# Performance work log

Measured on AMD Instinct MI355X. Metric: run time of the kernel, lower is better.

Reference implementation:

```python
import jax, jax.numpy as jnp
import numpy as np

MD = 4  # max_displacement
NEG_SLOPE = 0.1  # LeakyReLU slope


def setup_inputs() -> dict:
    key = jax.random.key(0)
    k1, k2 = jax.random.split(key)
    B, H, W, C = 8, 128, 192, 128
    x1 = jax.random.normal(k1, (B, H, W, C), dtype=jnp.float32)
    warped = jax.random.normal(k2, (B, H, W, C), dtype=jnp.float32)
    return {"x1": x1, "warped": warped}


def reference(x1, warped):
    # cost[b,h,w,k] = mean_c x1[b,h,w,c] * warped[b,h+sh,w+sw,c]  (zero-padded)
    # k enumerates (sh, sw) in row-major order over [-MD, MD] x [-MD, MD].
    md = MD
    B, H, W, C = x1.shape
    wp = jnp.pad(warped, ((0, 0), (md, md), (md, md), (0, 0)))
    cv = []
    for sh in range(-md, md + 1):
        for sw in range(-md, md + 1):
            shifted = jax.lax.dynamic_slice(wp, (0, md + sh, md + sw, 0), (B, H, W, C))
            cv.append(jnp.mean(x1 * shifted, axis=3))
    cv = jnp.stack(cv, axis=3)  # [B, H, W, (2*md+1)**2]
    return jnp.where(cv >= 0, cv, NEG_SLOPE * cv)
```

## Files before the change

### kernel.cpp

```cpp
#include <hip/hip_runtime.h>


namespace {
constexpr int Bb = 8, Hh = 128, Ww = 192, Cn = 128;
constexpr int MDc = 4;
constexpr int TH = 8, TWT = 16;
constexpr int NTHR = 512;
constexpr int RH = 16;
constexpr int RPX = 24;
constexpr int KC = 32;
constexpr int NCH = Cn / KC;
constexpr int KQB = RPX * 16;
constexpr int ROWB = 4 * KQB;
constexpr int BUFB = RH * ROWB;
constexpr int RUNS = RH * RPX * 4;
constexpr int NIT = RUNS / NTHR;
constexpr float NEG = 0.1f;
}

typedef __fp16 h2v   __attribute__((ext_vector_type(2)));
typedef __fp16 f16x8 __attribute__((ext_vector_type(8)));
typedef float  f32x4 __attribute__((ext_vector_type(4)));

__device__ __forceinline__ unsigned pkh2(float a, float b) {
    h2v h = __builtin_amdgcn_cvt_pkrtz(a, b);
    return __builtin_bit_cast(unsigned, h);
}

__device__ __forceinline__ void barrier_lgkm() {
    asm volatile("s_waitcnt lgkmcnt(0)\n\ts_barrier" ::: "memory");
}

__global__ __launch_bounds__(NTHR, 4)
void costvol_mfma(const float* __restrict__ x1,
                  const float* __restrict__ wp,
                  float* __restrict__ out)
{
    __shared__ __align__(16) unsigned char smem[2 * BUFB];

    const int tid  = threadIdx.x;
    const int wv   = tid >> 6;
    const int lane = tid & 63;
    const int nI   = lane & 15;
    const int kq   = lane >> 4;

    const int id = blockIdx.x;
    const int wg = (id & 7) * 192 + (id >> 3);
    const int bx = wg % 12;
    const int t2 = wg / 12;
    const int by = t2 & 15;
    const int bz = t2 >> 4;

    const int w0 = bx * TWT;
    const int h0 = by * TH;
    const int b  = bz;

    int g_off[NIT]; int l_off[NIT]; bool g_ok[NIT];
#pragma unroll
    for (int it = 0; it < NIT; ++it) {
        int s   = tid + it * NTHR;
        int skq = s & 3;
        int t   = s >> 2;
        int px  = t % RPX;
        int row = t / RPX;
        int hw  = h0 - MDc + row;
        int ww  = w0 - MDc + px;
        bool ok = (unsigned)hw < (unsigned)Hh && (unsigned)ww < (unsigned)Ww;
        g_ok[it]  = ok;
        g_off[it] = ((b * Hh + (ok ? hw : 0)) * Ww + (ok ? ww : 0)) * Cn + skq * 8;
        l_off[it] = row * ROWB + skq * KQB + ((px ^ (skq << 1)) * 16);
    }

    uint4 gp[NIT];
    auto LOADCH = [&](int ch) {
#pragma unroll
        for (int it = 0; it < NIT; ++it) {
            if (g_ok[it]) {
                const float* p = wp + g_off[it] + ch * KC;
                float4 u = *reinterpret_cast<const float4*>(p);
                float4 v = *reinterpret_cast<const float4*>(p + 4);
                gp[it] = make_uint4(pkh2(u.x, u.y), pkh2(u.z, u.w),
                                    pkh2(v.x, v.y), pkh2(v.z, v.w));
            } else {
                gp[it] = make_uint4(0u, 0u, 0u, 0u);
            }
        }
    };
    auto WRITEB = [&](int buf) {
#pragma unroll
        for (int it = 0; it < NIT; ++it)
            *reinterpret_cast<uint4*>(smem + buf * BUFB + l_off[it]) = gp[it];
    };

    LOADCH(0);

    const float* xp = x1 + ((size_t)((b * Hh + h0 + wv) * Ww) + w0 + nI) * Cn + kq * 8;
    float4 ar_u, ar_v;
    ar_u = *reinterpret_cast<const float4*>(xp);
    ar_v = *reinterpret_cast<const float4*>(xp + 4);

    f32x4 ac0[9], ac1[9];
#pragma unroll
    for (int s = 0; s < 9; ++s) {
        f32x4 z = {0.f, 0.f, 0.f, 0.f};
        ac0[s] = z; ac1[s] = z;
    }

    const int ro0 = kq * KQB + ((nI ^ (kq << 1)) * 16);

    WRITEB(0); LOADCH(1);

    int cur = 0;
#pragma unroll
    for (int ch = 0; ch < NCH; ++ch) {
        barrier_lgkm();
        if (ch + 1 < NCH) WRITEB(cur ^ 1);
        if (ch + 2 < NCH) LOADCH(ch + 2);
        uint4 afr = make_uint4(pkh2(ar_u.x, ar_u.y), pkh2(ar_u.z, ar_u.w),
                               pkh2(ar_v.x, ar_v.y), pkh2(ar_v.z, ar_v.w));
        if (ch + 1 < NCH) {
            ar_u = *reinterpret_cast<const float4*>(xp + (ch + 1) * KC);
            ar_v = *reinterpret_cast<const float4*>(xp + (ch + 1) * KC + 4);
        }
        f16x8 av = __builtin_bit_cast(f16x8, afr);
        const unsigned char* base = smem + cur * BUFB;
#pragma unroll
        for (int sh = 0; sh < 9; ++sh) {
            const unsigned char* rp = base + (wv + sh) * ROWB;
            uint4 b0 = *reinterpret_cast<const uint4*>(rp + ro0);
            uint4 b1 = *reinterpret_cast<const uint4*>(rp + ro0 + 128);
            ac0[sh] = __builtin_amdgcn_mfma_f32_16x16x32_f16(
                av, __builtin_bit_cast(f16x8, b0), ac0[sh], 0, 0, 0);
            ac1[sh] = __builtin_amdgcn_mfma_f32_16x16x32_f16(
                av, __builtin_bit_cast(f16x8, b1), ac1[sh], 0, 0, 0);
        }
        cur ^= 1;
    }

    const float sc = 1.0f / (float)Cn;
    const size_t rowbase = ((size_t)((b * Hh + h0 + wv) * Ww) + w0) * 81;
#pragma unroll
    for (int rg = 0; rg < 4; ++rg) {
        int m = kq * 4 + rg;
        int d = nI - m;
        bool t0 = (d >= 0 && d <= 8);
        bool t1 = (d >= -8 && d <= 0 && nI >= 8);
        size_t mb = rowbase + (size_t)m * 81;
#pragma unroll
        for (int sh = 0; sh < 9; ++sh) {
            if (t0) {
                float v = ac0[sh][rg] * sc;
                v = (v >= 0.f) ? v : NEG * v;
                out[mb + sh * 9 + d] = v;
            }
            if (t1) {
                float v = ac1[sh][rg] * sc;
                v = (v >= 0.f) ? v : NEG * v;
                out[mb + sh * 9 + d + 8] = v;
            }
        }
    }
}

extern "C" void kernel_launch(void* const* d_in, const int* in_sizes, int n_in,
                              void* d_out, int out_size, void* d_ws, size_t ws_size,
                              hipStream_t stream) {
    const float* x1 = (const float*)d_in[0];
    const float* wp = (const float*)d_in[1];
    float* out = (float*)d_out;
    dim3 grid(12 * 16 * 8, 1, 1);
    costvol_mfma<<<grid, NTHR, 0, stream>>>(x1, wp, out);
}
```

Measured before the change: 59.65 us.

## Halve tile height and split vertical shifts across wave pairs

Tile height drops from 8 to 4 output rows, so the grid doubles. Each pair of waves now shares one output row, with one wave handling 5 vertical shifts and the other 4. The per-wave accumulator count falls from 18 to 10 MFMA tiles, which lowers register pressure and halves the shared-memory buffer, and so may raise occupancy and parallelism. In exchange, each block reloads a larger halo relative to its output (12 rows loaded for 4 output rows, against 16 for 8), which adds global-memory traffic. The two waves of a pair also do unequal work.

```diff
diff --git a/kernel.cpp b/kernel.cpp
--- a/kernel.cpp
+++ b/kernel.cpp
@@ -4,9 +4,9 @@
 namespace {
 constexpr int Bb = 8, Hh = 128, Ww = 192, Cn = 128;
 constexpr int MDc = 4;
-constexpr int TH = 8, TWT = 16;
+constexpr int TH = 4, TWT = 16;
 constexpr int NTHR = 512;
-constexpr int RH = 16;
+constexpr int RH = TH + 8;
 constexpr int RPX = 24;
 constexpr int KC = 32;
 constexpr int NCH = Cn / KC;
@@ -14,7 +14,7 @@
 constexpr int ROWB = 4 * KQB;
 constexpr int BUFB = RH * ROWB;
 constexpr int RUNS = RH * RPX * 4;
-constexpr int NIT = RUNS / NTHR;
+constexpr int NIT = 3;
 constexpr float NEG = 0.1f;
 }
 
@@ -39,17 +39,20 @@
     __shared__ __align__(16) unsigned char smem[2 * BUFB];
 
     const int tid  = threadIdx.x;
-    const int wv   = tid >> 6;
+    const int w    = tid >> 6;
+    const int wvr  = w >> 1;
+    const int shb  = (w & 1) * 5;
+    const int shn  = 5 - (w & 1);
     const int lane = tid & 63;
     const int nI   = lane & 15;
     const int kq   = lane >> 4;
 
     const int id = blockIdx.x;
-    const int wg = (id & 7) * 192 + (id >> 3);
+    const int wg = (id & 7) * 384 + (id >> 3);
     const int bx = wg % 12;
     const int t2 = wg / 12;
-    const int by = t2 & 15;
-    const int bz = t2 >> 4;
+    const int by = t2 & 31;
+    const int bz = t2 >> 5;
 
     const int w0 = bx * TWT;
     const int h0 = by * TH;
@@ -65,7 +68,8 @@
         int row = t / RPX;
         int hw  = h0 - MDc + row;
         int ww  = w0 - MDc + px;
-        bool ok = (unsigned)hw < (unsigned)Hh && (unsigned)ww < (unsigned)Ww;
+        bool ok = (s < RUNS) &&
+                  (unsigned)hw < (unsigned)Hh && (unsigned)ww < (unsigned)Ww;
         g_ok[it]  = ok;
         g_off[it] = ((b * Hh + (ok ? hw : 0)) * Ww + (ok ? ww : 0)) * Cn + skq * 8;
         l_off[it] = row * ROWB + skq * KQB + ((px ^ (skq << 1)) * 16);
@@ -87,21 +91,22 @@
         }
     };
     auto WRITEB = [&](int buf) {
-#pragma unroll
-        for (int it = 0; it < NIT; ++it)
-            *reinterpret_cast<uint4*>(smem + buf * BUFB + l_off[it]) = gp[it];
+        *reinterpret_cast<uint4*>(smem + buf * BUFB + l_off[0]) = gp[0];
+        *reinterpret_cast<uint4*>(smem + buf * BUFB + l_off[1]) = gp[1];
+        if (tid < RUNS - 2 * NTHR)
+            *reinterpret_cast<uint4*>(smem + buf * BUFB + l_off[2]) = gp[2];
     };
 
     LOADCH(0);
 
-    const float* xp = x1 + ((size_t)((b * Hh + h0 + wv) * Ww) + w0 + nI) * Cn + kq * 8;
+    const float* xp = x1 + ((size_t)((b * Hh + h0 + wvr) * Ww) + w0 + nI) * Cn + kq * 8;
     float4 ar_u, ar_v;
     ar_u = *reinterpret_cast<const float4*>(xp);
     ar_v = *reinterpret_cast<const float4*>(xp + 4);
 
-    f32x4 ac0[9], ac1[9];
+    f32x4 ac0[5], ac1[5];
 #pragma unroll
-    for (int s = 0; s < 9; ++s) {
+    for (int s = 0; s < 5; ++s) {
         f32x4 z = {0.f, 0.f, 0.f, 0.f};
         ac0[s] = z; ac1[s] = z;
     }
@@ -125,38 +130,42 @@
         f16x8 av = __builtin_bit_cast(f16x8, afr);
         const unsigned char* base = smem + cur * BUFB;
 #pragma unroll
-        for (int sh = 0; sh < 9; ++sh) {
-            const unsigned char* rp = base + (wv + sh) * ROWB;
-            uint4 b0 = *reinterpret_cast<const uint4*>(rp + ro0);
-            uint4 b1 = *reinterpret_cast<const uint4*>(rp + ro0 + 128);
-            ac0[sh] = __builtin_amdgcn_mfma_f32_16x16x32_f16(
-                av, __builtin_bit_cast(f16x8, b0), ac0[sh], 0, 0, 0);
-            ac1[sh] = __builtin_amdgcn_mfma_f32_16x16x32_f16(
-                av, __builtin_bit_cast(f16x8, b1), ac1[sh], 0, 0, 0);
+        for (int s = 0; s < 5; ++s) {
+            if (s < shn) {
+                const unsigned char* rp = base + (wvr + shb + s) * ROWB;
+                uint4 b0 = *reinterpret_cast<const uint4*>(rp + ro0);
+                uint4 b1 = *reinterpret_cast<const uint4*>(rp + ro0 + 128);
+                ac0[s] = __builtin_amdgcn_mfma_f32_16x16x32_f16(
+                    av, __builtin_bit_cast(f16x8, b0), ac0[s], 0, 0, 0);
+                ac1[s] = __builtin_amdgcn_mfma_f32_16x16x32_f16(
+                    av, __builtin_bit_cast(f16x8, b1), ac1[s], 0, 0, 0);
+            }
         }
         cur ^= 1;
     }
 
     const float sc = 1.0f / (float)Cn;
-    const size_t rowbase = ((size_t)((b * Hh + h0 + wv) * Ww) + w0) * 81;
+    const size_t rowbase = ((size_t)((b * Hh + h0 + wvr) * Ww) + w0) * 81;
 #pragma unroll
     for (int rg = 0; rg < 4; ++rg) {
         int m = kq * 4 + rg;
         int d = nI - m;
         bool t0 = (d >= 0 && d <= 8);
         bool t1 = (d >= -8 && d <= 0 && nI >= 8);
-        size_t mb = rowbase + (size_t)m * 81;
+        size_t mb = rowbase + (size_t)m * 81 + shb * 9;
 #pragma unroll
-        for (int sh = 0; sh < 9; ++sh) {
-            if (t0) {
-                float v = ac0[sh][rg] * sc;
-                v = (v >= 0.f) ? v : NEG * v;
-                out[mb + sh * 9 + d] = v;
-            }
-            if (t1) {
-                float v = ac1[sh][rg] * sc;
-                v = (v >= 0.f) ? v : NEG * v;
-                out[mb + sh * 9 + d + 8] = v;
+        for (int s = 0; s < 5; ++s) {
+            if (s < shn) {
+                if (t0) {
+                    float v = ac0[s][rg] * sc;
+                    v = (v >= 0.f) ? v : NEG * v;
+                    out[mb + s * 9 + d] = v;
+                }
+                if (t1) {
+                    float v = ac1[s][rg] * sc;
+                    v = (v >= 0.f) ? v : NEG * v;
+                    out[mb + s * 9 + d + 8] = v;
+                }
             }
         }
     }
@@ -168,6 +177,6 @@
     const float* x1 = (const float*)d_in[0];
     const float* wp = (const float*)d_in[1];
     float* out = (float*)d_out;
-    dim3 grid(12 * 16 * 8, 1, 1);
+    dim3 grid(12 * 32 * 8, 1, 1);
     costvol_mfma<<<grid, NTHR, 0, stream>>>(x1, wp, out);
 }
```

Measured after the change: 66.61 us. 1.12x slower.

## Make blocks persistent over three tiles with cross-tile prefetch pipelining

Applied to the files above, without the earlier changes.

Each block now processes three consecutive tiles instead of one, with the grid shrunk from 1536 to 512 blocks. The loads of the first chunks of the next tile are issued during the last chunks of the current tile, so global-load latency is overlapped across tile boundaries and per-block launch/prologue cost is amortized. The trade-off is fewer blocks, which reduces parallelism and occupancy slack for the 256 CUs (two blocks per CU), and adds register pressure from keeping the next tile's offsets live.

```diff
diff --git a/kernel.cpp b/kernel.cpp
--- a/kernel.cpp
+++ b/kernel.cpp
@@ -15,6 +15,7 @@
 constexpr int BUFB = RH * ROWB;
 constexpr int RUNS = RH * RPX * 4;
 constexpr int NIT = RUNS / NTHR;
+constexpr int NTILE = 3;
 constexpr float NEG = 0.1f;
 }
 
@@ -44,32 +45,36 @@
     const int nI   = lane & 15;
     const int kq   = lane >> 4;
 
-    const int id = blockIdx.x;
-    const int wg = (id & 7) * 192 + (id >> 3);
-    const int bx = wg % 12;
-    const int t2 = wg / 12;
-    const int by = t2 & 15;
-    const int bz = t2 >> 4;
-
-    const int w0 = bx * TWT;
-    const int h0 = by * TH;
-    const int b  = bz;
-
-    int g_off[NIT]; int l_off[NIT]; bool g_ok[NIT];
+    const int kb = blockIdx.x;
+    int wg = (kb & 7) * 192 + (kb >> 3) * NTILE;
+
+    int w0, h0, b;
+    {
+        int bx = wg % 12, t2 = wg / 12;
+        w0 = bx * TWT; h0 = (t2 & 15) * TH; b = t2 >> 4;
+    }
+
+    int l_off[NIT];
 #pragma unroll
     for (int it = 0; it < NIT; ++it) {
-        int s   = tid + it * NTHR;
-        int skq = s & 3;
-        int t   = s >> 2;
-        int px  = t % RPX;
-        int row = t / RPX;
-        int hw  = h0 - MDc + row;
-        int ww  = w0 - MDc + px;
-        bool ok = (unsigned)hw < (unsigned)Hh && (unsigned)ww < (unsigned)Ww;
-        g_ok[it]  = ok;
-        g_off[it] = ((b * Hh + (ok ? hw : 0)) * Ww + (ok ? ww : 0)) * Cn + skq * 8;
+        int s = tid + it * NTHR, skq = s & 3, t = s >> 2;
+        int px = t % RPX, row = t / RPX;
         l_off[it] = row * ROWB + skq * KQB + ((px ^ (skq << 1)) * 16);
     }
+
+    int g_off[NIT]; bool g_ok[NIT];
+    auto OFFS = [&](int tw0, int th0, int tb) {
+#pragma unroll
+        for (int it = 0; it < NIT; ++it) {
+            int s = tid + it * NTHR, skq = s & 3, t = s >> 2;
+            int px = t % RPX, row = t / RPX;
+            int hw = th0 - MDc + row, ww = tw0 - MDc + px;
+            bool ok = (unsigned)hw < (unsigned)Hh && (unsigned)ww < (unsigned)Ww;
+            g_ok[it]  = ok;
+            g_off[it] = ((tb * Hh + (ok ? hw : 0)) * Ww + (ok ? ww : 0)) * Cn + skq * 8;
+        }
+    };
+    OFFS(w0, h0, b);
 
     uint4 gp[NIT];
     auto LOADCH = [&](int ch) {
@@ -95,9 +100,8 @@
     LOADCH(0);
 
     const float* xp = x1 + ((size_t)((b * Hh + h0 + wv) * Ww) + w0 + nI) * Cn + kq * 8;
-    float4 ar_u, ar_v;
-    ar_u = *reinterpret_cast<const float4*>(xp);
-    ar_v = *reinterpret_cast<const float4*>(xp + 4);
+    float4 ar_u = *reinterpret_cast<const float4*>(xp);
+    float4 ar_v = *reinterpret_cast<const float4*>(xp + 4);
 
     f32x4 ac0[9], ac1[9];
 #pragma unroll
@@ -110,54 +114,80 @@
 
     WRITEB(0); LOADCH(1);
 
-    int cur = 0;
-#pragma unroll
-    for (int ch = 0; ch < NCH; ++ch) {
-        barrier_lgkm();
-        if (ch + 1 < NCH) WRITEB(cur ^ 1);
-        if (ch + 2 < NCH) LOADCH(ch + 2);
-        uint4 afr = make_uint4(pkh2(ar_u.x, ar_u.y), pkh2(ar_u.z, ar_u.w),
-                               pkh2(ar_v.x, ar_v.y), pkh2(ar_v.z, ar_v.w));
-        if (ch + 1 < NCH) {
-            ar_u = *reinterpret_cast<const float4*>(xp + (ch + 1) * KC);
-            ar_v = *reinterpret_cast<const float4*>(xp + (ch + 1) * KC + 4);
-        }
-        f16x8 av = __builtin_bit_cast(f16x8, afr);
-        const unsigned char* base = smem + cur * BUFB;
-#pragma unroll
-        for (int sh = 0; sh < 9; ++sh) {
-            const unsigned char* rp = base + (wv + sh) * ROWB;
-            uint4 b0 = *reinterpret_cast<const uint4*>(rp + ro0);
-            uint4 b1 = *reinterpret_cast<const uint4*>(rp + ro0 + 128);
-            ac0[sh] = __builtin_amdgcn_mfma_f32_16x16x32_f16(
-                av, __builtin_bit_cast(f16x8, b0), ac0[sh], 0, 0, 0);
-            ac1[sh] = __builtin_amdgcn_mfma_f32_16x16x32_f16(
-                av, __builtin_bit_cast(f16x8, b1), ac1[sh], 0, 0, 0);
-        }
-        cur ^= 1;
-    }
-
+    int nw0 = w0, nh0 = h0, nb = b;
+    const float* xpn = xp;
     const float sc = 1.0f / (float)Cn;
-    const size_t rowbase = ((size_t)((b * Hh + h0 + wv) * Ww) + w0) * 81;
-#pragma unroll
-    for (int rg = 0; rg < 4; ++rg) {
-        int m = kq * 4 + rg;
-        int d = nI - m;
-        bool t0 = (d >= 0 && d <= 8);
-        bool t1 = (d >= -8 && d <= 0 && nI >= 8);
-        size_t mb = rowbase + (size_t)m * 81;
-#pragma unroll
-        for (int sh = 0; sh < 9; ++sh) {
-            if (t0) {
-                float v = ac0[sh][rg] * sc;
-                v = (v >= 0.f) ? v : NEG * v;
-                out[mb + sh * 9 + d] = v;
-            }
-            if (t1) {
-                float v = ac1[sh][rg] * sc;
-                v = (v >= 0.f) ? v : NEG * v;
-                out[mb + sh * 9 + d + 8] = v;
-            }
+
+    for (int t = 0; t < NTILE; ++t) {
+        const bool hn = (t + 1 < NTILE);
+#pragma unroll
+        for (int ch = 0; ch < NCH; ++ch) {
+            barrier_lgkm();
+            if (ch != 3 || hn) WRITEB((ch & 1) ^ 1);
+            if (ch == 0) LOADCH(2);
+            if (ch == 1) LOADCH(3);
+            if (ch == 2 && hn) {
+                int wgn = wg + 1;
+                int bx = wgn % 12, t2 = wgn / 12;
+                nw0 = bx * TWT; nh0 = (t2 & 15) * TH; nb = t2 >> 4;
+                OFFS(nw0, nh0, nb);
+                xpn = x1 + ((size_t)((nb * Hh + nh0 + wv) * Ww) + nw0 + nI) * Cn + kq * 8;
+                LOADCH(0);
+            }
+            if (ch == 3 && hn) LOADCH(1);
+            uint4 afr = make_uint4(pkh2(ar_u.x, ar_u.y), pkh2(ar_u.z, ar_u.w),
+                                   pkh2(ar_v.x, ar_v.y), pkh2(ar_v.z, ar_v.w));
+            if (ch < 3) {
+                ar_u = *reinterpret_cast<const float4*>(xp + (ch + 1) * KC);
+                ar_v = *reinterpret_cast<const float4*>(xp + (ch + 1) * KC + 4);
+            } else if (hn) {
+                ar_u = *reinterpret_cast<const float4*>(xpn);
+                ar_v = *reinterpret_cast<const float4*>(xpn + 4);
+            }
+            f16x8 av = __builtin_bit_cast(f16x8, afr);
+            const unsigned char* base = smem + (ch & 1) * BUFB;
+#pragma unroll
+            for (int sh = 0; sh < 9; ++sh) {
+                const unsigned char* rp = base + (wv + sh) * ROWB;
+                uint4 b0 = *reinterpret_cast<const uint4*>(rp + ro0);
+                uint4 b1 = *reinterpret_cast<const uint4*>(rp + ro0 + 128);
+                ac0[sh] = __builtin_amdgcn_mfma_f32_16x16x32_f16(
+                    av, __builtin_bit_cast(f16x8, b0), ac0[sh], 0, 0, 0);
+                ac1[sh] = __builtin_amdgcn_mfma_f32_16x16x32_f16(
+                    av, __builtin_bit_cast(f16x8, b1), ac1[sh], 0, 0, 0);
+            }
+        }
+
+        const size_t rowbase = ((size_t)((b * Hh + h0 + wv) * Ww) + w0) * 81;
+#pragma unroll
+        for (int rg = 0; rg < 4; ++rg) {
+            int m = kq * 4 + rg;
+            int d = nI - m;
+            bool t0 = (d >= 0 && d <= 8);
+            bool t1 = (d >= -8 && d <= 0 && nI >= 8);
+            size_t mb = rowbase + (size_t)m * 81;
+#pragma unroll
+            for (int sh = 0; sh < 9; ++sh) {
+                if (t0) {
+                    float v = ac0[sh][rg] * sc;
+                    v = (v >= 0.f) ? v : NEG * v;
+                    out[mb + sh * 9 + d] = v;
+                }
+                if (t1) {
+                    float v = ac1[sh][rg] * sc;
+                    v = (v >= 0.f) ? v : NEG * v;
+                    out[mb + sh * 9 + d + 8] = v;
+                }
+            }
+        }
+
+        if (hn) {
+#pragma unroll
+            for (int s = 0; s < 9; ++s) {
+                f32x4 z = {0.f, 0.f, 0.f, 0.f};
+                ac0[s] = z; ac1[s] = z;
+            }
+            w0 = nw0; h0 = nh0; b = nb; xp = xpn; ++wg;
         }
     }
 }
@@ -168,6 +198,6 @@
     const float* x1 = (const float*)d_in[0];
     const float* wp = (const float*)d_in[1];
     float* out = (float*)d_out;
-    dim3 grid(12 * 16 * 8, 1, 1);
+    dim3 grid(512, 1, 1);
     costvol_mfma<<<grid, NTHR, 0, stream>>>(x1, wp, out);
 }
```

Measured after the change: 140.0 us. +134.6%, slower.
